# Kernel tuning notes

Hardware: AMD Instinct MI355X
Metric: run time of the kernel (lower is better)

## Reference

```python
import jax, jax.numpy as jnp
import numpy as np

B = 8192
E, IN, H, OUT = 6, 2086, 512, 512


def setup_inputs() -> dict:
    key = jax.random.key(0)
    ks = jax.random.split(key, 6)
    wb1 = np.sqrt(6.0 / (IN * H))
    wb2 = np.sqrt(6.0 / (H * H))
    wb3 = np.sqrt(6.0 / (H * OUT))
    return {
        "frame_prev": jax.random.normal(ks[0], (B, 1830), dtype=jnp.float32),
        "I": jax.random.normal(ks[1], (B, 256), dtype=jnp.float32),
        "blending_coef": jax.nn.softmax(jax.random.normal(ks[2], (B, E), dtype=jnp.float32), axis=-1),
        "w1": jax.random.uniform(ks[3], (E, IN, H), jnp.float32, -wb1, wb1),
        "b1": jnp.zeros((E, H), jnp.float32),
        "w2": jax.random.uniform(ks[4], (E, H, H), jnp.float32, -wb2, wb2),
        "b2": jnp.zeros((E, H), jnp.float32),
        "w3": jax.random.uniform(ks[5], (E, H, OUT), jnp.float32, -wb3, wb3),
        "b3": jnp.zeros((E, OUT), jnp.float32),
    }


def _blended_linear(h, coef, w, b):
    # Algebraically identical to sum_e coef[b,e] * (h @ w[e]) + coef @ b,
    # which equals (h @ sum_e coef[b,e] w[e]) + coef @ b as in the torch code,
    # but avoids materializing the [B, in, out] blended weight tensor.
    per_expert = jnp.einsum('bi,eio->beo', h, w)   # [B, E, out]
    return jnp.einsum('be,beo->bo', coef, per_expert) + coef @ b


def reference(frame_prev, I, blending_coef, w1, b1, w2, b2, w3, b3):
    h0 = jnp.concatenate([frame_prev, I], axis=1)          # [B, 2086]
    h1 = jax.nn.elu(_blended_linear(h0, blending_coef, w1, b1))
    h2 = jax.nn.elu(_blended_linear(h1, blending_coef, w2, b2))
    h3 = jax.nn.elu(_blended_linear(h2, blending_coef, w3, b3))
    return h3
```

## Files before the change

kernel.cpp:

```cpp
#include <hip/hip_runtime.h>
#include <hip/hip_bf16.h>
#include <cstdint>
#include <cstddef>

typedef __attribute__((ext_vector_type(4))) float f32x4;
typedef __attribute__((ext_vector_type(8))) short bf16x8;

#define E_  6
#define B_  8192
#define H_  512

__device__ __forceinline__ unsigned short f32_to_bf16_rn(float f) {
    uint32_t u = __float_as_uint(f);
    uint32_t r = (u + 0x7fffu + ((u >> 16) & 1u)) >> 16;
    return (unsigned short)r;
}
__device__ __forceinline__ float bf16_to_f32(unsigned short h) {
    return __uint_as_float(((uint32_t)h) << 16);
}

__global__ void convert_h_kernel(const float* __restrict__ srcA, const float* __restrict__ srcB,
                                 int splitA, int K_in, int NK, int nchunks,
                                 short* __restrict__ dhi, short* __restrict__ dlo)
{
    int c = blockIdx.x * 256 + threadIdx.x;
    if (c >= nchunks) return;
    int lane  = c & 63;
    int mf    = (c >> 6) & 7;
    int rest  = c >> 9;
    int kstep = rest % NK;
    int bm    = rest / NK;
    int b  = bm * 128 + mf * 16 + (lane & 15);
    int k0 = kstep * 32 + (lane >> 4) * 8;

    union { short s[8]; int4 v; } uh, ul;
#pragma unroll
    for (int j = 0; j < 8; ++j) {
        int k = k0 + j;
        float v = 0.f;
        if (k < K_in) {
            v = (k < splitA) ? srcA[(size_t)b * splitA + k]
                             : srcB[(size_t)b * (K_in - splitA) + (k - splitA)];
        }
        unsigned short h = f32_to_bf16_rn(v);
        float rem = v - bf16_to_f32(h);
        unsigned short l = f32_to_bf16_rn(rem);
        uh.s[j] = (short)h;
        ul.s[j] = (short)l;
    }
    *reinterpret_cast<int4*>(dhi + (size_t)c * 8) = uh.v;
    *reinterpret_cast<int4*>(dlo + (size_t)c * 8) = ul.v;
}

__global__ void convert_w_kernel(const float* __restrict__ w, int K_in, int NK, int nchunks,
                                 short* __restrict__ dhi, short* __restrict__ dlo)
{
    int c = blockIdx.x * 256 + threadIdx.x;
    if (c >= nchunks) return;
    int lane  = c & 63;
    int nf    = (c >> 6) & 3;
    int rest  = c >> 8;
    int kstep = rest % NK;
    int eb    = rest / NK;
    int bn    = eb & 7;
    int e     = eb >> 3;
    int o  = bn * 64 + nf * 16 + (lane & 15);
    int k0 = kstep * 32 + (lane >> 4) * 8;

    union { short s[8]; int4 v; } uh, ul;
#pragma unroll
    for (int j = 0; j < 8; ++j) {
        int k = k0 + j;
        float v = 0.f;
        if (k < K_in) v = w[((size_t)e * K_in + k) * H_ + o];
        unsigned short h = f32_to_bf16_rn(v);
        float rem = v - bf16_to_f32(h);
        unsigned short l = f32_to_bf16_rn(rem);
        uh.s[j] = (short)h;
        ul.s[j] = (short)l;
    }
    *reinterpret_cast<int4*>(dhi + (size_t)c * 8) = uh.v;
    *reinterpret_cast<int4*>(dlo + (size_t)c * 8) = ul.v;
}

__global__ __launch_bounds__(256, 2)
void blend_gemm_kernel(const short* __restrict__ Ah, const short* __restrict__ Al,
                       const short* __restrict__ Bh, const short* __restrict__ Bl,
                       const float* __restrict__ coef, const float* __restrict__ bias,
                       float* __restrict__ out, int NK)
{
    __shared__ __align__(16) short lds[24576];

    const int tid  = threadIdx.x;
    const int lane = tid & 63;
    const int wave = tid >> 6;
    const int wm   = wave >> 1;
    const int wn   = wave & 1;
    const int blk  = blockIdx.x;
    const int bn   = blk & 7;
    const int bm   = blk >> 3;

    const size_t abase     = (size_t)bm * NK * 4096;
    const size_t bstride_e = (size_t)8 * NK * 2048;
    const size_t bbase0    = (size_t)bn * NK * 2048;

    auto issueA = [&](int s) {
        const size_t a_s = abase + (size_t)s * 4096;
        short* dst = &lds[(s & 1) * 8192];
#pragma unroll
        for (int i = 0; i < 4; ++i) {
            const int ch = wave * 4 + i;
            const short* g = (ch < 8) ? (Ah + a_s + ch * 512)
                                      : (Al + a_s + (ch - 8) * 512);
            __builtin_amdgcn_global_load_lds(
                (const __attribute__((address_space(1))) short*)(g + lane * 8),
                (__attribute__((address_space(3))) short*)(dst + ch * 512),
                16, 0, 0);
        }
    };
    auto issueB = [&](int e, int s) {
        const size_t off = (size_t)e * bstride_e + bbase0 + (size_t)s * 2048;
        short* dst = &lds[16384 + (e & 1) * 4096];
#pragma unroll
        for (int i = 0; i < 2; ++i) {
            const int ch = wave * 2 + i;
            const short* g = (ch < 4) ? (Bh + off + ch * 512)
                                      : (Bl + off + (ch - 4) * 512);
            __builtin_amdgcn_global_load_lds(
                (const __attribute__((address_space(1))) short*)(g + lane * 8),
                (__attribute__((address_space(3))) short*)(dst + ch * 512),
                16, 0, 0);
        }
    };

    const f32x4 zero = {0.f, 0.f, 0.f, 0.f};
    f32x4 acc[E_][4][2];
#pragma unroll
    for (int e = 0; e < E_; ++e)
#pragma unroll
        for (int mf = 0; mf < 4; ++mf)
#pragma unroll
            for (int nf = 0; nf < 2; ++nf) acc[e][mf][nf] = zero;

    bf16x8 ah[4], al4[4];

    issueA(0);
    issueB(0, 0);

    for (int s = 0; s < NK; ++s) {
        const bool last = (s == NK - 1);
#pragma unroll
        for (int e = 0; e < 6; ++e) {
            if (e < 4) {
                issueB(e + 1, s);
            } else if (e == 4) {
                issueB(5, s);
                if (!last) issueA(s + 1);
            } else {
                if (!last) issueB(0, s + 1);
            }
            if (e < 4) {
                asm volatile("s_waitcnt vmcnt(2)" ::: "memory");
            } else if (e == 4) {
                if (!last) asm volatile("s_waitcnt vmcnt(6)" ::: "memory");
                else       asm volatile("s_waitcnt vmcnt(2)" ::: "memory");
            } else {
                if (!last) asm volatile("s_waitcnt vmcnt(6)" ::: "memory");
                else       asm volatile("s_waitcnt vmcnt(0)" ::: "memory");
            }
            __builtin_amdgcn_s_barrier();
            __builtin_amdgcn_sched_barrier(0);

            if (e == 0) {
                const short* Ab = &lds[(s & 1) * 8192];
#pragma unroll
                for (int mf = 0; mf < 4; ++mf) {
                    ah[mf]  = *reinterpret_cast<const bf16x8*>(&Ab[((wm * 4 + mf) * 64 + lane) * 8]);
                    al4[mf] = *reinterpret_cast<const bf16x8*>(&Ab[((8 + wm * 4 + mf) * 64 + lane) * 8]);
                }
            }
            const short* Bb = &lds[16384 + (e & 1) * 4096];
            bf16x8 bh[2], bl[2];
#pragma unroll
            for (int nf = 0; nf < 2; ++nf) {
                bh[nf] = *reinterpret_cast<const bf16x8*>(&Bb[((wn * 2 + nf) * 64 + lane) * 8]);
                bl[nf] = *reinterpret_cast<const bf16x8*>(&Bb[((4 + wn * 2 + nf) * 64 + lane) * 8]);
            }

            __builtin_amdgcn_s_setprio(1);
#pragma unroll
            for (int mf = 0; mf < 4; ++mf)
#pragma unroll
                for (int nf = 0; nf < 2; ++nf) {
                    acc[e][mf][nf] = __builtin_amdgcn_mfma_f32_16x16x32_bf16(ah[mf],  bh[nf], acc[e][mf][nf], 0, 0, 0);
                    acc[e][mf][nf] = __builtin_amdgcn_mfma_f32_16x16x32_bf16(ah[mf],  bl[nf], acc[e][mf][nf], 0, 0, 0);
                    acc[e][mf][nf] = __builtin_amdgcn_mfma_f32_16x16x32_bf16(al4[mf], bh[nf], acc[e][mf][nf], 0, 0, 0);
                }
            __builtin_amdgcn_s_setprio(0);
            __builtin_amdgcn_sched_barrier(0);
            __builtin_amdgcn_s_barrier();
        }
    }

    float bb[E_][2];
#pragma unroll
    for (int nf = 0; nf < 2; ++nf) {
        const int col = bn * 64 + wn * 32 + nf * 16 + (lane & 15);
#pragma unroll
        for (int e = 0; e < E_; ++e) bb[e][nf] = bias[e * H_ + col];
    }

#pragma unroll
    for (int mf = 0; mf < 4; ++mf) {
        const int r0 = bm * 128 + wm * 64 + mf * 16 + (lane >> 4) * 4;
#pragma unroll
        for (int q = 0; q < 4; ++q) {
            const int r = r0 + q;
            const float2* c2 = reinterpret_cast<const float2*>(coef + (size_t)r * E_);
            float2 ca = c2[0], cb = c2[1], cc = c2[2];
            float cf[E_] = {ca.x, ca.y, cb.x, cb.y, cc.x, cc.y};
#pragma unroll
            for (int nf = 0; nf < 2; ++nf) {
                const int col = bn * 64 + wn * 32 + nf * 16 + (lane & 15);
                float v = 0.f;
#pragma unroll
                for (int e = 0; e < E_; ++e)
                    v += cf[e] * (acc[e][mf][nf][q] + bb[e][nf]);
                v = v > 0.f ? v : expm1f(v);
                out[(size_t)r * H_ + col] = v;
            }
        }
    }
}

extern "C" void kernel_launch(void* const* d_in, const int* in_sizes, int n_in,
                              void* d_out, int out_size, void* d_ws, size_t ws_size,
                              hipStream_t stream)
{
    if (n_in < 9) return;
    const float* frame = (const float*)d_in[0];
    const float* Iin   = (const float*)d_in[1];
    const float* coef  = (const float*)d_in[2];
    const float* w1    = (const float*)d_in[3];
    const float* b1    = (const float*)d_in[4];
    const float* w2    = (const float*)d_in[5];
    const float* b2    = (const float*)d_in[6];
    const float* w3    = (const float*)d_in[7];
    const float* b3    = (const float*)d_in[8];
    float* out = (float*)d_out;
    char* ws = (char*)d_ws;

    const int NK1 = 66;
    const int NK2 = 16;

    const size_t A0sz = (size_t)8192 * 2112 * 2;
    const size_t W1sz = (size_t)6 * 2112 * 512 * 2;
    const size_t W2sz = (size_t)6 * 512 * 512 * 2;
    const size_t H1f  = (size_t)8192 * 512 * 4;
    const size_t H1b  = (size_t)8192 * 512 * 2;

    const size_t need = 2 * A0sz + 2 * W1sz + 4 * W2sz + H1f + 2 * H1b;
    if (ws_size < need) return;

    short* A0h = (short*)(ws);
    short* A0l = (short*)(ws + A0sz);
    short* w1h = (short*)(ws + 2 * A0sz);
    short* w1l = (short*)(ws + 2 * A0sz + W1sz);
    short* w2h = (short*)(ws + 2 * A0sz + 2 * W1sz);
    short* w2l = (short*)(ws + 2 * A0sz + 2 * W1sz + W2sz);
    short* w3h = (short*)(ws + 2 * A0sz + 2 * W1sz + 2 * W2sz);
    short* w3l = (short*)(ws + 2 * A0sz + 2 * W1sz + 3 * W2sz);
    float* h1  = (float*)(ws + 2 * A0sz + 2 * W1sz + 4 * W2sz);
    short* h1h = (short*)((char*)h1 + H1f);
    short* h1l = (short*)((char*)h1 + H1f + H1b);
    float* h2  = (float*)(ws);
    short* h2h = (short*)(ws + H1f);
    short* h2l = (short*)(ws + H1f + H1b);

    {
        int nch = (8192 / 128) * NK1 * 8 * 64;
        convert_h_kernel<<<nch / 256, 256, 0, stream>>>(frame, Iin, 1830, 2086, NK1, nch, A0h, A0l);
    }
    {
        int nch = 6 * 8 * NK1 * 4 * 64;
        convert_w_kernel<<<nch / 256, 256, 0, stream>>>(w1, 2086, NK1, nch, w1h, w1l);
    }
    {
        int nch = 6 * 8 * NK2 * 4 * 64;
        convert_w_kernel<<<nch / 256, 256, 0, stream>>>(w2, 512, NK2, nch, w2h, w2l);
        convert_w_kernel<<<nch / 256, 256, 0, stream>>>(w3, 512, NK2, nch, w3h, w3l);
    }

    const int grid = 512;
    blend_gemm_kernel<<<grid, 256, 0, stream>>>(A0h, A0l, w1h, w1l, coef, b1, h1, NK1);
    {
        int nch = (8192 / 128) * NK2 * 8 * 64;
        convert_h_kernel<<<nch / 256, 256, 0, stream>>>(h1, nullptr, 512, 512, NK2, nch, h1h, h1l);
    }
    blend_gemm_kernel<<<grid, 256, 0, stream>>>(h1h, h1l, w2h, w2l, coef, b2, h2, NK2);
    {
        int nch = (8192 / 128) * NK2 * 8 * 64;
        convert_h_kernel<<<nch / 256, 256, 0, stream>>>(h2, nullptr, 512, 512, NK2, nch, h2h, h2l);
    }
    blend_gemm_kernel<<<grid, 256, 0, stream>>>(h2h, h2l, w3h, w3l, coef, b3, out, NK2);
}
```

Before: 602.1 us.

## Switch to 32x32x16 MFMA with triple-buffered expert B tiles

Changes the blended GEMM from 16x16x32 to 32x32x16 bf16 MFMA tiles and rewrites the hi/lo A and B packing kernels to match the new fragment layout. The B-tile LDS ring grows from two to three buffers so each expert's weights are prefetched two steps ahead, and the trailing barrier per expert step is removed. The aim is fewer MFMA and LDS-read instructions per FLOP and more load/compute overlap. The cost is more LDS per block and a new epilogue row mapping that must match the 32x32 accumulator layout.

```diff
diff --git a/kernel.cpp b/kernel.cpp
--- a/kernel.cpp
+++ b/kernel.cpp
@@ -3,8 +3,9 @@
 #include <cstdint>
 #include <cstddef>
 
-typedef __attribute__((ext_vector_type(4))) float f32x4;
-typedef __attribute__((ext_vector_type(8))) short bf16x8;
+typedef __attribute__((ext_vector_type(4)))  float f32x4;
+typedef __attribute__((ext_vector_type(16))) float f32x16;
+typedef __attribute__((ext_vector_type(8)))  short bf16x8;
 
 #define E_  6
 #define B_  8192
@@ -26,12 +27,14 @@
     int c = blockIdx.x * 256 + threadIdx.x;
     if (c >= nchunks) return;
     int lane  = c & 63;
-    int mf    = (c >> 6) & 7;
+    int ca    = (c >> 6) & 7;
     int rest  = c >> 9;
     int kstep = rest % NK;
     int bm    = rest / NK;
-    int b  = bm * 128 + mf * 16 + (lane & 15);
-    int k0 = kstep * 32 + (lane >> 4) * 8;
+    int mf32  = ca >> 1;
+    int ksub  = ca & 1;
+    int b  = bm * 128 + mf32 * 32 + (lane & 31);
+    int k0 = kstep * 32 + ksub * 16 + (lane >> 5) * 8;
 
     union { short s[8]; int4 v; } uh, ul;
 #pragma unroll
@@ -58,14 +61,16 @@
     int c = blockIdx.x * 256 + threadIdx.x;
     if (c >= nchunks) return;
     int lane  = c & 63;
-    int nf    = (c >> 6) & 3;
+    int ca    = (c >> 6) & 3;
     int rest  = c >> 8;
     int kstep = rest % NK;
     int eb    = rest / NK;
     int bn    = eb & 7;
     int e     = eb >> 3;
-    int o  = bn * 64 + nf * 16 + (lane & 15);
-    int k0 = kstep * 32 + (lane >> 4) * 8;
+    int nf32  = ca >> 1;
+    int ksub  = ca & 1;
+    int o  = bn * 64 + nf32 * 32 + (lane & 31);
+    int k0 = kstep * 32 + ksub * 16 + (lane >> 5) * 8;
 
     union { short s[8]; int4 v; } uh, ul;
 #pragma unroll
@@ -89,7 +94,7 @@
                        const float* __restrict__ coef, const float* __restrict__ bias,
                        float* __restrict__ out, int NK)
 {
-    __shared__ __align__(16) short lds[24576];
+    __shared__ __align__(16) short lds[28672];
 
     const int tid  = threadIdx.x;
     const int lane = tid & 63;
@@ -118,9 +123,9 @@
                 16, 0, 0);
         }
     };
-    auto issueB = [&](int e, int s) {
-        const size_t off = (size_t)e * bstride_e + bbase0 + (size_t)s * 2048;
-        short* dst = &lds[16384 + (e & 1) * 4096];
+    auto issueB = [&](int ebuf, int eexp, int s) {
+        const size_t off = (size_t)eexp * bstride_e + bbase0 + (size_t)s * 2048;
+        short* dst = &lds[16384 + ebuf * 4096];
 #pragma unroll
         for (int i = 0; i < 2; ++i) {
             const int ch = wave * 2 + i;
@@ -133,102 +138,100 @@
         }
     };
 
-    const f32x4 zero = {0.f, 0.f, 0.f, 0.f};
-    f32x4 acc[E_][4][2];
+    f32x16 acc[E_][2];
 #pragma unroll
     for (int e = 0; e < E_; ++e)
 #pragma unroll
-        for (int mf = 0; mf < 4; ++mf)
-#pragma unroll
-            for (int nf = 0; nf < 2; ++nf) acc[e][mf][nf] = zero;
-
-    bf16x8 ah[4], al4[4];
-
+        for (int mf = 0; mf < 2; ++mf)
+#pragma unroll
+            for (int q = 0; q < 16; ++q) acc[e][mf][q] = 0.f;
+
+    bf16x8 ah[2][2], al4[2][2];
+
+    __builtin_amdgcn_sched_barrier(0);
     issueA(0);
-    issueB(0, 0);
+    issueB(0, 0, 0);
+    issueB(1, 1, 0);
+    __builtin_amdgcn_sched_barrier(0);
 
     for (int s = 0; s < NK; ++s) {
-        const bool last = (s == NK - 1);
+        const bool lastS = (s == NK - 1);
 #pragma unroll
         for (int e = 0; e < 6; ++e) {
             if (e < 4) {
-                issueB(e + 1, s);
+                asm volatile("s_waitcnt vmcnt(2) lgkmcnt(0)" ::: "memory");
             } else if (e == 4) {
-                issueB(5, s);
-                if (!last) issueA(s + 1);
+                if (!lastS) asm volatile("s_waitcnt vmcnt(6) lgkmcnt(0)" ::: "memory");
+                else        asm volatile("s_waitcnt vmcnt(2) lgkmcnt(0)" ::: "memory");
             } else {
-                if (!last) issueB(0, s + 1);
-            }
-            if (e < 4) {
-                asm volatile("s_waitcnt vmcnt(2)" ::: "memory");
-            } else if (e == 4) {
-                if (!last) asm volatile("s_waitcnt vmcnt(6)" ::: "memory");
-                else       asm volatile("s_waitcnt vmcnt(2)" ::: "memory");
-            } else {
-                if (!last) asm volatile("s_waitcnt vmcnt(6)" ::: "memory");
-                else       asm volatile("s_waitcnt vmcnt(0)" ::: "memory");
+                if (!lastS) asm volatile("s_waitcnt vmcnt(6) lgkmcnt(0)" ::: "memory");
+                else        asm volatile("s_waitcnt vmcnt(0) lgkmcnt(0)" ::: "memory");
             }
             __builtin_amdgcn_s_barrier();
             __builtin_amdgcn_sched_barrier(0);
 
+            if (e < 4) {
+                issueB((e + 2) % 3, e + 2, s);
+            } else if (!lastS) {
+                issueB((e + 2) % 3, e - 4, s + 1);
+            }
+            if (e == 3 && !lastS) issueA(s + 1);
+            __builtin_amdgcn_sched_barrier(0);
+
             if (e == 0) {
                 const short* Ab = &lds[(s & 1) * 8192];
 #pragma unroll
-                for (int mf = 0; mf < 4; ++mf) {
-                    ah[mf]  = *reinterpret_cast<const bf16x8*>(&Ab[((wm * 4 + mf) * 64 + lane) * 8]);
-                    al4[mf] = *reinterpret_cast<const bf16x8*>(&Ab[((8 + wm * 4 + mf) * 64 + lane) * 8]);
-                }
+                for (int mf = 0; mf < 2; ++mf)
+#pragma unroll
+                    for (int ks = 0; ks < 2; ++ks) {
+                        const int ca = (wm * 2 + mf) * 2 + ks;
+                        ah[mf][ks]  = *reinterpret_cast<const bf16x8*>(&Ab[(ca * 64 + lane) * 8]);
+                        al4[mf][ks] = *reinterpret_cast<const bf16x8*>(&Ab[((8 + ca) * 64 + lane) * 8]);
+                    }
             }
-            const short* Bb = &lds[16384 + (e & 1) * 4096];
+            const short* Bb = &lds[16384 + (e % 3) * 4096];
             bf16x8 bh[2], bl[2];
 #pragma unroll
-            for (int nf = 0; nf < 2; ++nf) {
-                bh[nf] = *reinterpret_cast<const bf16x8*>(&Bb[((wn * 2 + nf) * 64 + lane) * 8]);
-                bl[nf] = *reinterpret_cast<const bf16x8*>(&Bb[((4 + wn * 2 + nf) * 64 + lane) * 8]);
+            for (int ks = 0; ks < 2; ++ks) {
+                const int cb = wn * 2 + ks;
+                bh[ks] = *reinterpret_cast<const bf16x8*>(&Bb[(cb * 64 + lane) * 8]);
+                bl[ks] = *reinterpret_cast<const bf16x8*>(&Bb[((4 + cb) * 64 + lane) * 8]);
             }
 
             __builtin_amdgcn_s_setprio(1);
 #pragma unroll
-            for (int mf = 0; mf < 4; ++mf)
-#pragma unroll
-                for (int nf = 0; nf < 2; ++nf) {
-                    acc[e][mf][nf] = __builtin_amdgcn_mfma_f32_16x16x32_bf16(ah[mf],  bh[nf], acc[e][mf][nf], 0, 0, 0);
-                    acc[e][mf][nf] = __builtin_amdgcn_mfma_f32_16x16x32_bf16(ah[mf],  bl[nf], acc[e][mf][nf], 0, 0, 0);
-                    acc[e][mf][nf] = __builtin_amdgcn_mfma_f32_16x16x32_bf16(al4[mf], bh[nf], acc[e][mf][nf], 0, 0, 0);
+            for (int ks = 0; ks < 2; ++ks)
+#pragma unroll
+                for (int mf = 0; mf < 2; ++mf) {
+                    acc[e][mf] = __builtin_amdgcn_mfma_f32_32x32x16_bf16(ah[mf][ks],  bh[ks], acc[e][mf], 0, 0, 0);
+                    acc[e][mf] = __builtin_amdgcn_mfma_f32_32x32x16_bf16(ah[mf][ks],  bl[ks], acc[e][mf], 0, 0, 0);
+                    acc[e][mf] = __builtin_amdgcn_mfma_f32_32x32x16_bf16(al4[mf][ks], bh[ks], acc[e][mf], 0, 0, 0);
                 }
             __builtin_amdgcn_s_setprio(0);
             __builtin_amdgcn_sched_barrier(0);
-            __builtin_amdgcn_s_barrier();
-        }
-    }
-
-    float bb[E_][2];
-#pragma unroll
-    for (int nf = 0; nf < 2; ++nf) {
-        const int col = bn * 64 + wn * 32 + nf * 16 + (lane & 15);
-#pragma unroll
-        for (int e = 0; e < E_; ++e) bb[e][nf] = bias[e * H_ + col];
-    }
-
-#pragma unroll
-    for (int mf = 0; mf < 4; ++mf) {
-        const int r0 = bm * 128 + wm * 64 + mf * 16 + (lane >> 4) * 4;
-#pragma unroll
-        for (int q = 0; q < 4; ++q) {
-            const int r = r0 + q;
+        }
+    }
+
+    const int col = bn * 64 + wn * 32 + (lane & 31);
+    float bb[E_];
+#pragma unroll
+    for (int e = 0; e < E_; ++e) bb[e] = bias[e * H_ + col];
+
+#pragma unroll
+    for (int mf = 0; mf < 2; ++mf) {
+#pragma unroll
+        for (int reg = 0; reg < 16; ++reg) {
+            const int row_local = (reg & 3) + 8 * (reg >> 2) + 4 * (lane >> 5);
+            const int r = bm * 128 + wm * 64 + mf * 32 + row_local;
             const float2* c2 = reinterpret_cast<const float2*>(coef + (size_t)r * E_);
-            float2 ca = c2[0], cb = c2[1], cc = c2[2];
-            float cf[E_] = {ca.x, ca.y, cb.x, cb.y, cc.x, cc.y};
-#pragma unroll
-            for (int nf = 0; nf < 2; ++nf) {
-                const int col = bn * 64 + wn * 32 + nf * 16 + (lane & 15);
-                float v = 0.f;
-#pragma unroll
-                for (int e = 0; e < E_; ++e)
-                    v += cf[e] * (acc[e][mf][nf][q] + bb[e][nf]);
-                v = v > 0.f ? v : expm1f(v);
-                out[(size_t)r * H_ + col] = v;
-            }
+            float2 ca = c2[0], cb2 = c2[1], cc = c2[2];
+            float cf[E_] = {ca.x, ca.y, cb2.x, cb2.y, cc.x, cc.y};
+            float v = 0.f;
+#pragma unroll
+            for (int e = 0; e < E_; ++e)
+                v += cf[e] * (acc[e][mf][reg] + bb[e]);
+            v = v > 0.f ? v : expm1f(v);
+            out[(size_t)r * H_ + col] = v;
         }
     }
 }
```

New measurement: 934.4 us. +55.2%, slower.

## Triple-buffer expert weight tiles in LDS and drop second per-step barrier

Applied to the files above, without the earlier changes.

Expands the B-operand LDS staging from two to three buffers so expert tiles are prefetched two steps ahead. Loads are now issued after the barrier, which lets the trailing barrier after the MFMA block be removed, so there is one barrier per expert step instead of two. The cost is more LDS per block, which could reduce occupancy, and correctness now relies on the new vmcnt accounting with A prefetch moved to e==3.

```diff
diff --git a/kernel.cpp b/kernel.cpp
--- a/kernel.cpp
+++ b/kernel.cpp
@@ -89,7 +89,7 @@
                        const float* __restrict__ coef, const float* __restrict__ bias,
                        float* __restrict__ out, int NK)
 {
-    __shared__ __align__(16) short lds[24576];
+    __shared__ __align__(16) short lds[28672];
 
     const int tid  = threadIdx.x;
     const int lane = tid & 63;
@@ -118,9 +118,9 @@
                 16, 0, 0);
         }
     };
-    auto issueB = [&](int e, int s) {
-        const size_t off = (size_t)e * bstride_e + bbase0 + (size_t)s * 2048;
-        short* dst = &lds[16384 + (e & 1) * 4096];
+    auto issueB = [&](int ebuf, int eexp, int s) {
+        const size_t off = (size_t)eexp * bstride_e + bbase0 + (size_t)s * 2048;
+        short* dst = &lds[16384 + ebuf * 4096];
 #pragma unroll
         for (int i = 0; i < 2; ++i) {
             const int ch = wave * 2 + i;
@@ -144,31 +144,34 @@
 
     bf16x8 ah[4], al4[4];
 
+    __builtin_amdgcn_sched_barrier(0);
     issueA(0);
-    issueB(0, 0);
+    issueB(0, 0, 0);
+    issueB(1, 1, 0);
+    __builtin_amdgcn_sched_barrier(0);
 
     for (int s = 0; s < NK; ++s) {
-        const bool last = (s == NK - 1);
+        const bool lastS = (s == NK - 1);
 #pragma unroll
         for (int e = 0; e < 6; ++e) {
             if (e < 4) {
-                issueB(e + 1, s);
+                asm volatile("s_waitcnt vmcnt(2) lgkmcnt(0)" ::: "memory");
             } else if (e == 4) {
-                issueB(5, s);
-                if (!last) issueA(s + 1);
+                if (!lastS) asm volatile("s_waitcnt vmcnt(6) lgkmcnt(0)" ::: "memory");
+                else        asm volatile("s_waitcnt vmcnt(2) lgkmcnt(0)" ::: "memory");
             } else {
-                if (!last) issueB(0, s + 1);
-            }
+                if (!lastS) asm volatile("s_waitcnt vmcnt(6) lgkmcnt(0)" ::: "memory");
+                else        asm volatile("s_waitcnt vmcnt(0) lgkmcnt(0)" ::: "memory");
+            }
+            __builtin_amdgcn_s_barrier();
+            __builtin_amdgcn_sched_barrier(0);
+
             if (e < 4) {
-                asm volatile("s_waitcnt vmcnt(2)" ::: "memory");
-            } else if (e == 4) {
-                if (!last) asm volatile("s_waitcnt vmcnt(6)" ::: "memory");
-                else       asm volatile("s_waitcnt vmcnt(2)" ::: "memory");
-            } else {
-                if (!last) asm volatile("s_waitcnt vmcnt(6)" ::: "memory");
-                else       asm volatile("s_waitcnt vmcnt(0)" ::: "memory");
-            }
-            __builtin_amdgcn_s_barrier();
+                issueB((e + 2) % 3, e + 2, s);
+            } else if (!lastS) {
+                issueB((e + 2) % 3, e - 4, s + 1);
+            }
+            if (e == 3 && !lastS) issueA(s + 1);
             __builtin_amdgcn_sched_barrier(0);
 
             if (e == 0) {
@@ -179,7 +182,7 @@
                     al4[mf] = *reinterpret_cast<const bf16x8*>(&Ab[((8 + wm * 4 + mf) * 64 + lane) * 8]);
                 }
             }
-            const short* Bb = &lds[16384 + (e & 1) * 4096];
+            const short* Bb = &lds[16384 + (e % 3) * 4096];
             bf16x8 bh[2], bl[2];
 #pragma unroll
             for (int nf = 0; nf < 2; ++nf) {
@@ -198,7 +201,6 @@
                 }
             __builtin_amdgcn_s_setprio(0);
             __builtin_amdgcn_sched_barrier(0);
-            __builtin_amdgcn_s_barrier();
         }
     }
 
```

Result: faster. 569.6 us (-5.4%).
